# Kernel optimization log

Measured on AMD Instinct MI355X. Metric: run time of the kernel, lower is better.

## Reference

```python
import jax, jax.numpy as jnp
import numpy as np

NEG_SLOPE = 0.01  # torch nn.LeakyReLU default
K_NN = 3          # PyG knn_interpolate default


def lrelu(v):
    return jax.nn.leaky_relu(v, NEG_SLOPE)


def mpl(x, ei, We, be, Wn, bn_):
    # MeshGraphNets-style message passing: edge MLP on [x_src||x_dst],
    # sum-aggregate at dst, node MLP on [x||agg].
    src, dst = ei[0], ei[1]
    m = lrelu(jnp.concatenate([x[src], x[dst]], axis=-1) @ We + be)   # [E, Co]
    agg = jax.ops.segment_sum(m, dst, num_segments=x.shape[0])        # [N, Co]
    return lrelu(jnp.concatenate([x, agg], axis=-1) @ Wn + bn_)


def knn_interpolate(x_c, pos_c, pos_f):
    # PyG knn_interpolate: inverse-squared-distance weighted k-NN average.
    d2 = jnp.sum((pos_f[:, None, :] - pos_c[None, :, :]) ** 2, axis=-1)  # [Nf, Nc]
    neg_d2, idx = jax.lax.top_k(-d2, K_NN)                               # [Nf, k]
    w = 1.0 / (-neg_d2 + 1e-16)
    xg = x_c[idx]                                                        # [Nf, k, C]
    return jnp.sum(w[..., None] * xg, axis=1) / jnp.sum(w, axis=1, keepdims=True)


def batch_norm(x, gamma, beta, eps=1e-5):
    # training-mode BatchNorm over the flattened node dim (PyG BatchNorm)
    mu = x.mean(axis=0)
    var = x.var(axis=0)
    return (x - mu) * jax.lax.rsqrt(var + eps) * gamma + beta


def setup_inputs() -> dict:
    key = jax.random.key(0)
    ks = jax.random.split(key, 20)
    B, Nc, Nf, D = 4, 2048, 8192, 3
    Cin, Cout = 128, 128
    Ch = Cout // 2
    Ec, Ef = 16384, 65536

    def w(k, shape):
        return jax.random.normal(k, shape, jnp.float32) / np.float32(np.sqrt(shape[0]))

    inp = {
        "x": jax.random.normal(ks[0], (B, Nc, Cin), jnp.float32),
        "weights": jax.random.uniform(ks[1], (B, Nc, 1), dtype=jnp.float32),
        "pos": jax.random.uniform(ks[2], (B, Nf, D), dtype=jnp.float32),
        # mpl1: Cin -> Cout//2 (coarse graph)
        "W1e": w(ks[3], (2 * Cin, Ch)), "b1e": jnp.zeros((Ch,), jnp.float32),
        "W1n": w(ks[4], (Cin + Ch, Ch)), "b1n": jnp.zeros((Ch,), jnp.float32),
        # mpl2: Cout//2 -> Cout (fine graph)
        "W2e": w(ks[5], (2 * Ch, Cout)), "b2e": jnp.zeros((Cout,), jnp.float32),
        "W2n": w(ks[6], (Ch + Cout, Cout)), "b2n": jnp.zeros((Cout,), jnp.float32),
        # mpl_skip: Cin -> Cout (fine graph)
        "Wse": w(ks[7], (2 * Cin, Cout)), "bse": jnp.zeros((Cout,), jnp.float32),
        "Wsn": w(ks[8], (Cin + Cout, Cout)), "bsn": jnp.zeros((Cout,), jnp.float32),
        "gamma": jnp.ones((Cout,), jnp.float32),
        "beta": jnp.zeros((Cout,), jnp.float32),
        # mask: indices of coarse nodes inside the fine node set (disjoint per graph)
        "mask": jnp.arange(B * Nc, dtype=jnp.int32).reshape(B, Nc),
        "e_coarse": jax.random.randint(ks[9], (B, 2, Ec), 0, Nc, jnp.int32),
        "e_fine": jax.random.randint(ks[10], (B, 2, Ef), 0, Nf, jnp.int32),
    }
    return inp


def reference(x, weights, pos, W1e, b1e, W1n, b1n, W2e, b2e, W2n, b2n,
              Wse, bse, Wsn, bsn, gamma, beta, mask, e_coarse, e_fine):
    B, Nf, _ = pos.shape

    def per_graph(xg, wg, posg, mg, ec, ef):
        pos_c = posg[mg]                                   # coarse positions
        # skip branch: up-pool then message passing on fine graph
        x_up = knn_interpolate(xg, pos_c, posg)            # [Nf, Cin]
        x_skip = mpl(x_up, ef, Wse, bse, Wsn, bsn)         # [Nf, Cout]
        # main branch: mpl on coarse graph, up-pool, mpl on fine graph
        x1 = mpl(xg, ec, W1e, b1e, W1n, b1n)               # [Nc, Cout//2]
        x1_up = knn_interpolate(x1, pos_c, posg)           # [Nf, Cout//2]
        x2 = mpl(x1_up, ef, W2e, b2e, W2n, b2n)            # [Nf, Cout]
        # Unpool node weights (scatter into zeros at mask rows)
        w_fine = jnp.zeros((Nf, wg.shape[-1]), wg.dtype).at[mg].set(wg)
        return x2 + x_skip, w_fine

    xs, w_fine = jax.vmap(per_graph)(x, weights, pos, mask, e_coarse, e_fine)
    C = xs.shape[-1]
    y = lrelu(batch_norm(xs.reshape(-1, C), gamma, beta)).reshape(xs.shape)
    return y, w_fine
```

## Files before the change

### kernel.cpp

```cpp
#include <hip/hip_runtime.h>
#include <hip/hip_bf16.h>
#include <cfloat>

#define B 4
#define NC 2048
#define NF 8192
#define CIN 128
#define CH 64
#define COUT 128
#define EC 16384
#define EF 65536
#define ZB 256

typedef __attribute__((ext_vector_type(8))) short short8v;
typedef __attribute__((ext_vector_type(4))) float f32x4;

__device__ __forceinline__ ushort f2b(float v) {
    __hip_bfloat16 h = __float2bfloat16(v);
    return *reinterpret_cast<ushort*>(&h);
}
__device__ __forceinline__ float b2f(ushort u) {
    __hip_bfloat16 h = *reinterpret_cast<__hip_bfloat16*>(&u);
    return __bfloat162float(h);
}

__global__ void count_all(const int* __restrict__ ec, const int* __restrict__ ef,
                          const int* __restrict__ mask, const float* __restrict__ pos,
                          int* __restrict__ cntC, int* __restrict__ cntF, int* __restrict__ cntZ) {
    const int b = blockIdx.y, z = blockIdx.z;
    const int i = blockIdx.x * 256 + threadIdx.x;
    if (z == 0) {
        if (i < EC) atomicAdd(&cntC[b * NC + ec[(size_t)b * 2 * EC + EC + i]], 1);
    } else if (z == 1) {
        if (i < EF) atomicAdd(&cntF[b * NF + ef[(size_t)b * 2 * EF + EF + i]], 1);
    } else {
        if (i < NC) {
            int m = mask[b * NC + i];
            float pz = pos[((size_t)b * NF + m) * 3 + 2];
            int zb = min(max((int)(pz * (float)ZB), 0), ZB - 1);
            atomicAdd(&cntZ[b * ZB + zb], 1);
        }
    }
}

template<int N, int OSTR, bool EXTRA>
__device__ __forceinline__ void scan_body(const int* __restrict__ cnt, int* __restrict__ offs,
                                          int* __restrict__ cur, int b, int* part) {
    const int tid = threadIdx.x;
    constexpr int PER = (N + 1023) / 1024;
    int local[PER];
    int s = 0;
    #pragma unroll
    for (int i = 0; i < PER; ++i) {
        int id = tid * PER + i;
        local[i] = s;
        if (id < N) s += cnt[b * N + id];
    }
    part[tid] = s;
    __syncthreads();
    for (int off = 1; off < 1024; off <<= 1) {
        int v = (tid >= off) ? part[tid - off] : 0;
        __syncthreads();
        part[tid] += v;
        __syncthreads();
    }
    int pre = tid ? part[tid - 1] : 0;
    #pragma unroll
    for (int i = 0; i < PER; ++i) {
        int id = tid * PER + i;
        if (id < N) {
            int o = pre + local[i];
            offs[b * OSTR + id] = o;
            cur[b * OSTR + id] = o;
        }
    }
    if (EXTRA && tid == 1023) offs[b * OSTR + N] = part[1023];
}

__global__ __launch_bounds__(1024) void scan_all(
    const int* __restrict__ cntC, int* __restrict__ offC, int* __restrict__ curC,
    const int* __restrict__ cntF, int* __restrict__ offF, int* __restrict__ curF,
    const int* __restrict__ cntZ, int* __restrict__ offZ, int* __restrict__ curZ) {
    __shared__ int part[1024];
    const int cfg = blockIdx.x >> 2;
    const int b = blockIdx.x & 3;
    if (cfg == 0)      scan_body<NC, NC, false>(cntC, offC, curC, b, part);
    else if (cfg == 1) scan_body<NF, NF, false>(cntF, offF, curF, b, part);
    else               scan_body<ZB, ZB + 1, true>(cntZ, offZ, curZ, b, part);
}

__global__ void fill_all(const int* __restrict__ ec, const int* __restrict__ ef,
                         const int* __restrict__ mask, const float* __restrict__ pos,
                         int* __restrict__ curC, int* __restrict__ curF, int* __restrict__ curZ,
                         int* __restrict__ csrC, int* __restrict__ csrF,
                         float4* __restrict__ sposg) {
    const int b = blockIdx.y, z = blockIdx.z;
    const int i = blockIdx.x * 256 + threadIdx.x;
    if (z == 0) {
        if (i < EC) {
            const int* eb = ec + (size_t)b * 2 * EC;
            int src = eb[i], dst = eb[EC + i];
            int p = atomicAdd(&curC[b * NC + dst], 1);
            csrC[(size_t)b * EC + p] = src;
        }
    } else if (z == 1) {
        if (i < EF) {
            const int* eb = ef + (size_t)b * 2 * EF;
            int src = eb[i], dst = eb[EF + i];
            int p = atomicAdd(&curF[b * NF + dst], 1);
            csrF[(size_t)b * EF + p] = src;
        }
    } else {
        if (i < NC) {
            int m = mask[b * NC + i];
            const float* p = pos + ((size_t)b * NF + m) * 3;
            float px = p[0], py = p[1], pz = p[2];
            int zb = min(max((int)(pz * (float)ZB), 0), ZB - 1);
            int slot = atomicAdd(&curZ[b * (ZB + 1) + zb], 1);
            sposg[(size_t)b * NC + slot] = make_float4(px, py, pz, __int_as_float(i));
        }
    }
}

__device__ __forceinline__ void ins3(float d, int c, float& d0, float& d1, float& d2,
                                     int& i0, int& i1, int& i2) {
    bool lt0 = d < d0, lt1 = d < d1, lt2 = d < d2;
    d2 = lt1 ? d1 : (lt2 ? d : d2);  i2 = lt1 ? i1 : (lt2 ? c : i2);
    d1 = lt0 ? d0 : (lt1 ? d : d1);  i1 = lt0 ? i0 : (lt1 ? c : i1);
    d0 = lt0 ? d  : d0;              i0 = lt0 ? c  : i0;
}
__device__ __forceinline__ void merge32(float& d0, float& d1, float& d2,
                                        int& i0, int& i1, int& i2) {
    #pragma unroll
    for (int off = 1; off <= 16; off <<= 1) {
        float od[3]; int oi[3];
        od[0] = __shfl_xor(d0, off); oi[0] = __shfl_xor(i0, off);
        od[1] = __shfl_xor(d1, off); oi[1] = __shfl_xor(i1, off);
        od[2] = __shfl_xor(d2, off); oi[2] = __shfl_xor(i2, off);
        #pragma unroll
        for (int j = 0; j < 3; ++j) ins3(od[j], oi[j], d0, d1, d2, i0, i1, i2);
    }
}

__global__ __launch_bounds__(256) void knn_interp(const float* __restrict__ pos,
                                                  const float4* __restrict__ sposg,
                                                  const int* __restrict__ offZ,
                                                  const float* __restrict__ xc,
                                                  int* __restrict__ idx,
                                                  float* __restrict__ wn,
                                                  ushort* __restrict__ xup) {
    const int b = blockIdx.y;
    const int tid = threadIdx.x;
    const int node = blockIdx.x * 8 + (tid >> 5);
    const int lane = tid & 31;
    const float* pf = pos + ((size_t)b * NF + node) * 3;
    const float px = pf[0], py = pf[1], pz = pf[2];
    const float4* sp = sposg + (size_t)b * NC;
    const int zb = min(max((int)(pz * (float)ZB), 0), ZB - 1);
    const int zlo = max(zb - 32, 0), zhi = min(zb + 32, ZB - 1);
    const int j0 = offZ[b * (ZB + 1) + zlo];
    const int j1 = offZ[b * (ZB + 1) + zhi + 1];
    float d0 = FLT_MAX, d1 = FLT_MAX, d2 = FLT_MAX;
    int i0 = 0, i1 = 0, i2 = 0;
    for (int j = j0 + lane; j < j1; j += 32) {
        float4 s = sp[j];
        float ddx = __fsub_rn(px, s.x);
        float ddy = __fsub_rn(py, s.y);
        float ddz = __fsub_rn(pz, s.z);
        float d = __fadd_rn(__fadd_rn(__fmul_rn(ddx, ddx), __fmul_rn(ddy, ddy)),
                            __fmul_rn(ddz, ddz));
        ins3(d, __float_as_int(s.w), d0, d1, d2, i0, i1, i2);
    }
    merge32(d0, d1, d2, i0, i1, i2);
    float bd = 1e30f;
    if (zlo > 0)      bd = fminf(bd, pz - (float)zlo * (1.0f / ZB));
    if (zhi < ZB - 1) bd = fminf(bd, (float)(zhi + 1) * (1.0f / ZB) - pz);
    bd *= 0.9999f;
    if (__any(d2 > bd * bd)) {
        d0 = d1 = d2 = FLT_MAX; i0 = i1 = i2 = 0;
        for (int j = lane; j < NC; j += 32) {
            float4 s = sp[j];
            float ddx = __fsub_rn(px, s.x);
            float ddy = __fsub_rn(py, s.y);
            float ddz = __fsub_rn(pz, s.z);
            float d = __fadd_rn(__fadd_rn(__fmul_rn(ddx, ddx), __fmul_rn(ddy, ddy)),
                                __fmul_rn(ddz, ddz));
            ins3(d, __float_as_int(s.w), d0, d1, d2, i0, i1, i2);
        }
        merge32(d0, d1, d2, i0, i1, i2);
    }
    float w0 = 1.0f / (d0 + 1e-16f);
    float w1 = 1.0f / (d1 + 1e-16f);
    float w2 = 1.0f / (d2 + 1e-16f);
    float inv = 1.0f / (w0 + w1 + w2);
    w0 *= inv; w1 *= inv; w2 *= inv;
    if (lane == 0) {
        size_t o = ((size_t)b * NF + node) * 3;
        idx[o] = i0; idx[o + 1] = i1; idx[o + 2] = i2;
        wn[o] = w0; wn[o + 1] = w1; wn[o + 2] = w2;
    }
    const float* xb = xc + (size_t)b * NC * CIN;
    float4 a = *(const float4*)&xb[(size_t)i0 * CIN + lane * 4];
    float4 bb = *(const float4*)&xb[(size_t)i1 * CIN + lane * 4];
    float4 cc = *(const float4*)&xb[(size_t)i2 * CIN + lane * 4];
    ushort4 u;
    u.x = f2b(w0 * a.x + w1 * bb.x + w2 * cc.x);
    u.y = f2b(w0 * a.y + w1 * bb.y + w2 * cc.y);
    u.z = f2b(w0 * a.z + w1 * bb.z + w2 * cc.z);
    u.w = f2b(w0 * a.w + w1 * bb.w + w2 * cc.w);
    *(ushort4*)&xup[((size_t)b * NF + node) * CIN + lane * 4] = u;
}

template<int S>
__global__ __launch_bounds__(256) void interp_b16(const float* __restrict__ xc,
                                                  const int* __restrict__ idx,
                                                  const float* __restrict__ wn,
                                                  ushort* __restrict__ out) {
    constexpr int C = 4 << S;
    const int b = blockIdx.y;
    const int node = blockIdx.x * (256 >> S) + (threadIdx.x >> S);
    const int lane = threadIdx.x & ((1 << S) - 1);
    size_t o = ((size_t)b * NF + node) * 3;
    int i0 = idx[o], i1 = idx[o + 1], i2 = idx[o + 2];
    float w0 = wn[o], w1 = wn[o + 1], w2 = wn[o + 2];
    const float* xb = xc + (size_t)b * NC * C;
    float4 a = *(const float4*)&xb[(size_t)i0 * C + lane * 4];
    float4 bb = *(const float4*)&xb[(size_t)i1 * C + lane * 4];
    float4 cc = *(const float4*)&xb[(size_t)i2 * C + lane * 4];
    ushort4 u;
    u.x = f2b(w0 * a.x + w1 * bb.x + w2 * cc.x);
    u.y = f2b(w0 * a.y + w1 * bb.y + w2 * cc.y);
    u.z = f2b(w0 * a.z + w1 * bb.z + w2 * cc.z);
    u.w = f2b(w0 * a.w + w1 * bb.w + w2 * cc.w);
    *(ushort4*)&out[((size_t)b * NF + node) * C + lane * 4] = u;
}

__global__ __launch_bounds__(256) void gemm_kernel(
    const float* __restrict__ A1, int K1, const float* __restrict__ A2, int K2,
    const float* __restrict__ W, const float* __restrict__ bias,
    float* __restrict__ Cmat, int M, int N, int flags,
    long sA1, long sA2, long sC) {
    __shared__ float As[16][64];
    __shared__ float Wsh[16][64];
    const int b = blockIdx.z;
    const int m0 = blockIdx.y * 64, n0 = blockIdx.x * 64;
    const int t = threadIdx.x;
    const int tx = t & 15, ty = t >> 4;
    float acc[4][4] = {};
    int kOff = 0;
    for (int s = 0; s < 2; ++s) {
        const float* A = (s == 0) ? A1 : A2;
        const int K = (s == 0) ? K1 : K2;
        const long sA = (s == 0) ? sA1 : sA2;
        if (A == nullptr || K == 0) continue;
        const float* Ab = A + (size_t)b * sA;
        const int lm = t >> 2;
        const int lk = (t & 3) << 2;
        const int wk = t >> 4;
        const int wng = (t & 15) << 2;
        for (int k0 = 0; k0 < K; k0 += 16) {
            float4 av = *(const float4*)&Ab[(size_t)(m0 + lm) * K + k0 + lk];
            As[lk + 0][lm] = av.x; As[lk + 1][lm] = av.y;
            As[lk + 2][lm] = av.z; As[lk + 3][lm] = av.w;
            float4 wv = *(const float4*)&W[(size_t)(kOff + k0 + wk) * N + n0 + wng];
            *(float4*)&Wsh[wk][wng] = wv;
            __syncthreads();
            #pragma unroll
            for (int k = 0; k < 16; ++k) {
                float4 a4 = *(const float4*)&As[k][ty << 2];
                float4 w4 = *(const float4*)&Wsh[k][tx << 2];
                float aa[4] = {a4.x, a4.y, a4.z, a4.w};
                float ww[4] = {w4.x, w4.y, w4.z, w4.w};
                #pragma unroll
                for (int i = 0; i < 4; ++i)
                    #pragma unroll
                    for (int j = 0; j < 4; ++j)
                        acc[i][j] = fmaf(aa[i], ww[j], acc[i][j]);
            }
            __syncthreads();
        }
        kOff += K;
    }
    float* Cb = Cmat + (size_t)b * sC;
    #pragma unroll
    for (int i = 0; i < 4; ++i) {
        int m = m0 + (ty << 2) + i;
        #pragma unroll
        for (int j = 0; j < 4; ++j) {
            int n = n0 + (tx << 2) + j;
            float v = acc[i][j];
            if (bias) v += bias[n];
            if (flags & 1) v = v > 0.0f ? v : 0.01f * v;
            float* cp = &Cb[(size_t)m * N + n];
            if (flags & 2) v += *cp;
            *cp = v;
        }
    }
}

__global__ __launch_bounds__(256) void gemm_pq64(const float* __restrict__ x,
                                                 const float* __restrict__ W1e,
                                                 float* __restrict__ Pb,
                                                 float* __restrict__ Qb) {
    __shared__ float As[16][64];
    __shared__ float Wsh[16][64];
    const int z = blockIdx.z;
    const int b = z >> 1, pq = z & 1;
    const int m0 = blockIdx.x * 64;
    const float* Ab = x + (size_t)b * NC * CIN;
    const float* W = W1e + pq * CIN * CH;
    float* Cb = (pq ? Qb : Pb) + (size_t)b * NC * CH;
    const int t = threadIdx.x;
    const int tx = t & 15, ty = t >> 4;
    const int lm = t >> 2, lk = (t & 3) << 2;
    const int wk = t >> 4, wng = (t & 15) << 2;
    float acc[4][4] = {};
    for (int k0 = 0; k0 < CIN; k0 += 16) {
        float4 av = *(const float4*)&Ab[(size_t)(m0 + lm) * CIN + k0 + lk];
        As[lk + 0][lm] = av.x; As[lk + 1][lm] = av.y;
        As[lk + 2][lm] = av.z; As[lk + 3][lm] = av.w;
        float4 wv = *(const float4*)&W[(size_t)(k0 + wk) * CH + wng];
        *(float4*)&Wsh[wk][wng] = wv;
        __syncthreads();
        #pragma unroll
        for (int k = 0; k < 16; ++k) {
            float4 a4 = *(const float4*)&As[k][ty << 2];
            float4 w4 = *(const float4*)&Wsh[k][tx << 2];
            float aa[4] = {a4.x, a4.y, a4.z, a4.w};
            float ww[4] = {w4.x, w4.y, w4.z, w4.w};
            #pragma unroll
            for (int i = 0; i < 4; ++i)
                #pragma unroll
                for (int j = 0; j < 4; ++j)
                    acc[i][j] = fmaf(aa[i], ww[j], acc[i][j]);
        }
        __syncthreads();
    }
    #pragma unroll
    for (int i = 0; i < 4; ++i) {
        int m = m0 + (ty << 2) + i;
        #pragma unroll
        for (int j = 0; j < 4; ++j)
            Cb[(size_t)m * CH + (tx << 2) + j] = acc[i][j];
    }
}

#define LDK 40
__device__ __forceinline__ void mfma_seg(const ushort* __restrict__ Ab, int K, int m0,
                                         const ushort* __restrict__ Wt, int ldW, int wcol0,
                                         ushort* As, ushort* Wsm,
                                         int t, int wr, int wc, int fr, int fq,
                                         f32x4 (&acc)[4][4]) {
    const int sr = t >> 2, sk = (t & 3) * 8;
    for (int k0 = 0; k0 < K; k0 += 32) {
        #pragma unroll
        for (int p = 0; p < 2; ++p) {
            int r = sr + p * 64;
            *reinterpret_cast<int4*>(&As[r * LDK + sk]) =
                *reinterpret_cast<const int4*>(&Ab[(size_t)(m0 + r) * K + k0 + sk]);
            *reinterpret_cast<int4*>(&Wsm[r * LDK + sk]) =
                *reinterpret_cast<const int4*>(&Wt[(size_t)r * ldW + wcol0 + k0 + sk]);
        }
        __syncthreads();
        short8v af[4], wf[4];
        #pragma unroll
        for (int m = 0; m < 4; ++m)
            af[m] = *reinterpret_cast<const short8v*>(&As[(wr * 64 + m * 16 + fr) * LDK + fq * 8]);
        #pragma unroll
        for (int n = 0; n < 4; ++n)
            wf[n] = *reinterpret_cast<const short8v*>(&Wsm[(wc * 64 + n * 16 + fr) * LDK + fq * 8]);
        #pragma unroll
        for (int m = 0; m < 4; ++m)
            #pragma unroll
            for (int n = 0; n < 4; ++n)
                acc[m][n] = __builtin_amdgcn_mfma_f32_16x16x32_bf16(af[m], wf[n], acc[m][n], 0, 0, 0);
        __syncthreads();
    }
}

__global__ __launch_bounds__(256) void mfma_pq_both(
    const ushort* __restrict__ x1upb, const ushort* __restrict__ xupb,
    const ushort* __restrict__ W2eT, const ushort* __restrict__ WseT,
    ushort* __restrict__ P2, ushort* __restrict__ Q2,
    ushort* __restrict__ PS, ushort* __restrict__ QS) {
    __shared__ ushort As[128 * LDK];
    __shared__ ushort Wsm[128 * LDK];
    const int t = threadIdx.x;
    const int lane = t & 63, wid = t >> 6;
    const int wr = wid >> 1, wc = wid & 1;
    const int fr = lane & 15, fq = lane >> 4;
    const int z = blockIdx.z;
    const int b = z >> 2, sel = z & 3;
    const int br = sel >> 1, pq = sel & 1;
    const int m0 = blockIdx.x * 128;
    f32x4 acc[4][4];
    #pragma unroll
    for (int m = 0; m < 4; ++m)
        #pragma unroll
        for (int n = 0; n < 4; ++n) acc[m][n] = (f32x4){0.f, 0.f, 0.f, 0.f};
    ushort* outp;
    if (br == 0) {
        mfma_seg(x1upb + (size_t)b * NF * 64, 64, m0, W2eT, 128, pq * 64,
                 As, Wsm, t, wr, wc, fr, fq, acc);
        outp = pq ? Q2 : P2;
    } else {
        mfma_seg(xupb + (size_t)b * NF * 128, 128, m0, WseT, 256, pq * 128,
                 As, Wsm, t, wr, wc, fr, fq, acc);
        outp = pq ? QS : PS;
    }
    ushort* Cb = outp + (size_t)b * NF * 128;
    #pragma unroll
    for (int m = 0; m < 4; ++m)
        #pragma unroll
        for (int n = 0; n < 4; ++n) {
            int col = wc * 64 + n * 16 + fr;
            #pragma unroll
            for (int r = 0; r < 4; ++r) {
                int row = m0 + wr * 64 + m * 16 + fq * 4 + r;
                Cb[(size_t)row * 128 + col] = f2b(acc[m][n][r]);
            }
        }
}

__global__ __launch_bounds__(256) void mfma_node2(
    const ushort* __restrict__ A1, const ushort* __restrict__ A2,
    const ushort* __restrict__ Wt1, const float* __restrict__ bias1,
    const ushort* __restrict__ A3, const ushort* __restrict__ A4,
    const ushort* __restrict__ Wt2, const float* __restrict__ bias2,
    float* __restrict__ y, float* __restrict__ stats) {
    __shared__ ushort As[128 * LDK];
    __shared__ ushort Wsm[128 * LDK];
    const int t = threadIdx.x;
    const int lane = t & 63, wid = t >> 6;
    const int wr = wid >> 1, wc = wid & 1;
    const int fr = lane & 15, fq = lane >> 4;
    const int b = blockIdx.z;
    const int m0 = blockIdx.x * 128;
    f32x4 acc1[4][4], acc2[4][4];
    #pragma unroll
    for (int m = 0; m < 4; ++m)
        #pragma unroll
        for (int n = 0; n < 4; ++n) {
            acc1[m][n] = (f32x4){0.f, 0.f, 0.f, 0.f};
            acc2[m][n] = (f32x4){0.f, 0.f, 0.f, 0.f};
        }
    mfma_seg(A1 + (size_t)b * NF * 64,  64,  m0, Wt1, 192, 0,   As, Wsm, t, wr, wc, fr, fq, acc1);
    mfma_seg(A2 + (size_t)b * NF * 128, 128, m0, Wt1, 192, 64,  As, Wsm, t, wr, wc, fr, fq, acc1);
    mfma_seg(A3 + (size_t)b * NF * 128, 128, m0, Wt2, 256, 0,   As, Wsm, t, wr, wc, fr, fq, acc2);
    mfma_seg(A4 + (size_t)b * NF * 128, 128, m0, Wt2, 256, 128, As, Wsm, t, wr, wc, fr, fq, acc2);
    float* Yb = y + (size_t)b * NF * 128;
    float lsum[4] = {0.f, 0.f, 0.f, 0.f}, lsq[4] = {0.f, 0.f, 0.f, 0.f};
    #pragma unroll
    for (int m = 0; m < 4; ++m)
        #pragma unroll
        for (int n = 0; n < 4; ++n) {
            int col = wc * 64 + n * 16 + fr;
            float bv1 = bias1[col], bv2 = bias2[col];
            #pragma unroll
            for (int r = 0; r < 4; ++r) {
                int row = m0 + wr * 64 + m * 16 + fq * 4 + r;
                float v1 = acc1[m][n][r] + bv1; v1 = v1 > 0.0f ? v1 : 0.01f * v1;
                float v2 = acc2[m][n][r] + bv2; v2 = v2 > 0.0f ? v2 : 0.01f * v2;
                float v = v1 + v2;
                Yb[(size_t)row * 128 + col] = v;
                lsum[n] += v;
                lsq[n] = fmaf(v, v, lsq[n]);
            }
        }
    __syncthreads();
    float* ssum = reinterpret_cast<float*>(As);
    float* ssq  = ssum + 128;
    if (t < 128) { ssum[t] = 0.0f; ssq[t] = 0.0f; }
    __syncthreads();
    #pragma unroll
    for (int n = 0; n < 4; ++n) {
        int col = wc * 64 + n * 16 + fr;
        atomicAdd(&ssum[col], lsum[n]);
        atomicAdd(&ssq[col], lsq[n]);
    }
    __syncthreads();
    if (t < 128) {
        atomicAdd(&stats[t], ssum[t]);
        atomicAdd(&stats[128 + t], ssq[t]);
    }
}

__global__ void conv_wt(const float* __restrict__ W2e, const float* __restrict__ W2n,
                        const float* __restrict__ Wse, const float* __restrict__ Wsn,
                        ushort* __restrict__ W2eT, ushort* __restrict__ W2nT,
                        ushort* __restrict__ WseT, ushort* __restrict__ WsnT) {
    const float* src; ushort* dst; int K2;
    switch (blockIdx.y) {
        case 0: src = W2e; dst = W2eT; K2 = 128; break;
        case 1: src = W2n; dst = W2nT; K2 = 192; break;
        case 2: src = Wse; dst = WseT; K2 = 256; break;
        default: src = Wsn; dst = WsnT; K2 = 256; break;
    }
    int id = blockIdx.x * 256 + threadIdx.x;
    if (id >= K2 * 128) return;
    int n = id & 127, k = id >> 7;
    dst[(size_t)n * K2 + k] = f2b(src[id]);
}

__global__ __launch_bounds__(256) void agg_csr_f32(const float* __restrict__ P,
                                                   const float* __restrict__ Q,
                                                   const float* __restrict__ bias,
                                                   const int* __restrict__ offs,
                                                   const int* __restrict__ counts,
                                                   const int* __restrict__ csr_src,
                                                   float* __restrict__ agg,
                                                   int N, int E) {
    const int b = blockIdx.y;
    const int dst = blockIdx.x * 4 + (threadIdx.x >> 6);
    const int lane = threadIdx.x & 63;
    const float* Pb = P + (size_t)b * N * 64;
    const float* Qb = Q + (size_t)b * N * 64;
    const int start = offs[b * N + dst];
    const int cnt = counts[b * N + dst];
    const int* sl = csr_src + (size_t)b * E + start;
    const float q = Qb[(size_t)dst * 64 + lane] + bias[lane];
    float a = 0.0f;
    for (int i = 0; i < cnt; ++i) {
        int src = sl[i];
        float m = Pb[(size_t)src * 64 + lane] + q; m = m > 0.0f ? m : 0.01f * m;
        a += m;
    }
    agg[(size_t)b * N * 64 + (size_t)dst * 64 + lane] = a;
}

__global__ __launch_bounds__(256) void agg_csr_b16(const ushort* __restrict__ P2,
                                                   const ushort* __restrict__ Q2,
                                                   const float* __restrict__ b2,
                                                   const ushort* __restrict__ PS,
                                                   const ushort* __restrict__ QS,
                                                   const float* __restrict__ bS,
                                                   const int* __restrict__ offs,
                                                   const int* __restrict__ counts,
                                                   const int* __restrict__ csr_src,
                                                   ushort* __restrict__ agg2,
                                                   ushort* __restrict__ aggS) {
    const int lin = blockIdx.x;
    const int pair = lin & 7;
    const int b = pair >> 1, br = pair & 1;
    const int chunk = lin >> 3;
    const ushort* P = br ? PS : P2;
    const ushort* Q = br ? QS : Q2;
    const float* bias = br ? bS : b2;
    ushort* agg = br ? aggS : agg2;
    const int dst = chunk * 4 + (threadIdx.x >> 6);
    const int lane = threadIdx.x & 63;
    const ushort* Pb = P + (size_t)b * NF * 128;
    const ushort* Qb = Q + (size_t)b * NF * 128;
    const int start = offs[b * NF + dst];
    const int cnt = counts[b * NF + dst];
    const int* sl = csr_src + (size_t)b * EF + start;
    const int c0 = lane, c1 = lane + 64;
    const float q0 = b2f(Qb[(size_t)dst * 128 + c0]) + bias[c0];
    const float q1 = b2f(Qb[(size_t)dst * 128 + c1]) + bias[c1];
    float a0 = 0.0f, a1 = 0.0f;
    int i = 0;
    for (; i + 4 <= cnt; i += 4) {
        int s0 = sl[i], s1 = sl[i + 1], s2 = sl[i + 2], s3 = sl[i + 3];
        ushort p00 = Pb[(size_t)s0 * 128 + c0], p01 = Pb[(size_t)s0 * 128 + c1];
        ushort p10 = Pb[(size_t)s1 * 128 + c0], p11 = Pb[(size_t)s1 * 128 + c1];
        ushort p20 = Pb[(size_t)s2 * 128 + c0], p21 = Pb[(size_t)s2 * 128 + c1];
        ushort p30 = Pb[(size_t)s3 * 128 + c0], p31 = Pb[(size_t)s3 * 128 + c1];
        float m;
        m = b2f(p00) + q0; m = m > 0.0f ? m : 0.01f * m; a0 += m;
        m = b2f(p01) + q1; m = m > 0.0f ? m : 0.01f * m; a1 += m;
        m = b2f(p10) + q0; m = m > 0.0f ? m : 0.01f * m; a0 += m;
        m = b2f(p11) + q1; m = m > 0.0f ? m : 0.01f * m; a1 += m;
        m = b2f(p20) + q0; m = m > 0.0f ? m : 0.01f * m; a0 += m;
        m = b2f(p21) + q1; m = m > 0.0f ? m : 0.01f * m; a1 += m;
        m = b2f(p30) + q0; m = m > 0.0f ? m : 0.01f * m; a0 += m;
        m = b2f(p31) + q1; m = m > 0.0f ? m : 0.01f * m; a1 += m;
    }
    for (; i < cnt; ++i) {
        int src = sl[i];
        float m0 = b2f(Pb[(size_t)src * 128 + c0]) + q0; m0 = m0 > 0.0f ? m0 : 0.01f * m0;
        float m1 = b2f(Pb[(size_t)src * 128 + c1]) + q1; m1 = m1 > 0.0f ? m1 : 0.01f * m1;
        a0 += m0; a1 += m1;
    }
    __builtin_nontemporal_store(f2b(a0), &agg[(size_t)b * NF * 128 + (size_t)dst * 128 + c0]);
    __builtin_nontemporal_store(f2b(a1), &agg[(size_t)b * NF * 128 + (size_t)dst * 128 + c1]);
}

__global__ __launch_bounds__(256) void bn_final(float* __restrict__ xs,
                                                const float* __restrict__ stats,
                                                const float* __restrict__ gamma,
                                                const float* __restrict__ beta,
                                                float* __restrict__ wf) {
    const long i = (long)blockIdx.x * 256 + threadIdx.x;
    const long g4 = i * 4;
    const int c = (int)(g4 & (COUT - 1));
    const float invN = 1.0f / (float)(B * NF);
    float4 v = *(float4*)&xs[g4];
    float vv[4] = {v.x, v.y, v.z, v.w};
    #pragma unroll
    for (int k = 0; k < 4; ++k) {
        int ck = c + k;
        float mu = stats[ck] * invN;
        float var = stats[COUT + ck] * invN - mu * mu;
        float t = (vv[k] - mu) * rsqrtf(var + 1e-5f) * gamma[ck] + beta[ck];
        vv[k] = t > 0.0f ? t : 0.01f * t;
    }
    *(float4*)&xs[g4] = make_float4(vv[0], vv[1], vv[2], vv[3]);
    if (i < (long)B * NF / 4)
        *(float4*)&wf[i * 4] = make_float4(0.f, 0.f, 0.f, 0.f);
}

__global__ void wfine_scatter(const float* __restrict__ wts, const int* __restrict__ mask,
                              float* __restrict__ wf) {
    int i = blockIdx.x * 256 + threadIdx.x;
    int b = i / NC;
    wf[(size_t)b * NF + mask[i]] = wts[i];
}

extern "C" void kernel_launch(void* const* d_in, const int* in_sizes, int n_in,
                              void* d_out, int out_size, void* d_ws, size_t ws_size,
                              hipStream_t stream) {
    const float* x    = (const float*)d_in[0];
    const float* wts  = (const float*)d_in[1];
    const float* pos  = (const float*)d_in[2];
    const float* W1e  = (const float*)d_in[3];
    const float* b1e  = (const float*)d_in[4];
    const float* W1n  = (const float*)d_in[5];
    const float* b1n  = (const float*)d_in[6];
    const float* W2e  = (const float*)d_in[7];
    const float* b2e  = (const float*)d_in[8];
    const float* W2n  = (const float*)d_in[9];
    const float* b2n  = (const float*)d_in[10];
    const float* Wse  = (const float*)d_in[11];
    const float* bse  = (const float*)d_in[12];
    const float* Wsn  = (const float*)d_in[13];
    const float* bsn  = (const float*)d_in[14];
    const float* gamma= (const float*)d_in[15];
    const float* beta = (const float*)d_in[16];
    const int*   mask = (const int*)d_in[17];
    const int*   ec   = (const int*)d_in[18];
    const int*   ef   = (const int*)d_in[19];

    float* ws = (float*)d_ws;
    int*    idxb  = (int*)ws;
    float*  wnb   = ws + 98304;
    float4* sposg = (float4*)(ws + 196608);
    float*  x1    = ws + 196608 + 32768;
    float*  PbC   = x1  + (size_t)B * NC * CH;
    float*  QbC   = PbC + (size_t)B * NC * CH;
    float*  aggC  = QbC + (size_t)B * NC * CH;
    float*  stats = aggC+ (size_t)B * NC * CH;
    int* cntC  = (int*)(stats + 256);
    int* cntF  = cntC + B * NC;
    int* cntZ  = cntF + B * NF;
    int* offC  = cntZ + B * ZB;
    int* curC  = offC + B * NC;
    int* offF  = curC + B * NC;
    int* curF  = offF + B * NF;
    int* offZ  = curF + B * NF;
    int* curZ  = offZ + B * (ZB + 1);
    int* csrC  = curZ + B * (ZB + 1);
    int* csrF  = csrC + B * EC;
    size_t foff = (size_t)(csrF + (size_t)B * EF - (int*)ws);
    foff = (foff + 7) & ~(size_t)7;
    ushort* xupb  = (ushort*)(ws + foff);
    ushort* x1upb = xupb  + (size_t)B * NF * 128;
    ushort* P2b   = x1upb + (size_t)B * NF * 64;
    ushort* Q2b   = P2b   + (size_t)B * NF * 128;
    ushort* PSb   = Q2b   + (size_t)B * NF * 128;
    ushort* QSb   = PSb   + (size_t)B * NF * 128;
    ushort* agg2b = QSb   + (size_t)B * NF * 128;
    ushort* aggSb = agg2b + (size_t)B * NF * 128;
    ushort* W2eT  = aggSb + (size_t)B * NF * 128;
    ushort* W2nT  = W2eT  + 128 * 128;
    ushort* WseT  = W2nT  + 128 * 192;
    ushort* WsnT  = WseT  + 128 * 256;

    float* y  = (float*)d_out;
    float* wf = y + (size_t)B * NF * COUT;

    conv_wt<<<dim3(128, 4), 256, 0, stream>>>(W2e, W2n, Wse, Wsn, W2eT, W2nT, WseT, WsnT);
    hipMemsetAsync(stats, 0, 256 * 4 + (size_t)B * (NC + NF + ZB) * 4, stream);
    count_all<<<dim3(EF / 256, B, 3), 256, 0, stream>>>(ec, ef, mask, pos, cntC, cntF, cntZ);
    scan_all<<<dim3(3 * B), 1024, 0, stream>>>(cntC, offC, curC, cntF, offF, curF, cntZ, offZ, curZ);
    fill_all<<<dim3(EF / 256, B, 3), 256, 0, stream>>>(ec, ef, mask, pos, curC, curF, curZ,
                                                       csrC, csrF, sposg);

    knn_interp<<<dim3(NF / 8, B), 256, 0, stream>>>(pos, sposg, offZ, x, idxb, wnb, xupb);

    gemm_pq64<<<dim3(NC / 64, 1, B * 2), 256, 0, stream>>>(x, W1e, PbC, QbC);
    agg_csr_f32<<<dim3(NC / 4, B), 256, 0, stream>>>(
        PbC, QbC, b1e, offC, cntC, csrC, aggC, NC, EC);
    gemm_kernel<<<dim3(1, NC / 64, B), 256, 0, stream>>>(
        x, CIN, aggC, CH, W1n, b1n, x1, NC, CH, 1, (long)NC * CIN, (long)NC * CH, (long)NC * CH);

    interp_b16<4><<<dim3(NF / 16, B), 256, 0, stream>>>(x1, idxb, wnb, x1upb);

    mfma_pq_both<<<dim3(NF / 128, 1, B * 4), 256, 0, stream>>>(
        x1upb, xupb, W2eT, WseT, P2b, Q2b, PSb, QSb);
    agg_csr_b16<<<dim3((NF / 4) * B * 2), 256, 0, stream>>>(
        P2b, Q2b, b2e, PSb, QSb, bse, offF, cntF, csrF, agg2b, aggSb);

    mfma_node2<<<dim3(NF / 128, 1, B), 256, 0, stream>>>(
        x1upb, agg2b, W2nT, b2n, xupb, aggSb, WsnT, bsn, y, stats);

    bn_final<<<dim3((long)B * NF * COUT / 1024), 256, 0, stream>>>(y, stats, gamma, beta, wf);
    wfine_scatter<<<dim3(B * NC / 256), 256, 0, stream>>>(wts, mask, wf);
}
```

Before: 197.2 us.

## Fold weight conversion and w_fine scatter into existing kernels; fuse P/Q GEMMs

Moves the weight transpose/bf16 conversion into an extra z-slice of count_all, and replaces the separate wfine_scatter kernel with an inverse mask map built in fill_all and consumed by bn_final. This removes two kernel launches. The edge-GEMM kernel now computes both the P and Q halves in one block, so each A tile is loaded once instead of twice. The cost is twice the accumulator registers and an extra shared-memory weight buffer, which may lower occupancy. The inverse map assumes mask entries are unique within a graph.

```diff
diff --git a/kernel.cpp b/kernel.cpp
--- a/kernel.cpp
+++ b/kernel.cpp
@@ -26,19 +26,37 @@
 
 __global__ void count_all(const int* __restrict__ ec, const int* __restrict__ ef,
                           const int* __restrict__ mask, const float* __restrict__ pos,
-                          int* __restrict__ cntC, int* __restrict__ cntF, int* __restrict__ cntZ) {
+                          int* __restrict__ cntC, int* __restrict__ cntF, int* __restrict__ cntZ,
+                          int* __restrict__ inv,
+                          const float* __restrict__ W2e, const float* __restrict__ W2n,
+                          const float* __restrict__ Wse, const float* __restrict__ Wsn,
+                          ushort* __restrict__ W2eT, ushort* __restrict__ W2nT,
+                          ushort* __restrict__ WseT, ushort* __restrict__ WsnT) {
     const int b = blockIdx.y, z = blockIdx.z;
     const int i = blockIdx.x * 256 + threadIdx.x;
     if (z == 0) {
         if (i < EC) atomicAdd(&cntC[b * NC + ec[(size_t)b * 2 * EC + EC + i]], 1);
     } else if (z == 1) {
         if (i < EF) atomicAdd(&cntF[b * NF + ef[(size_t)b * 2 * EF + EF + i]], 1);
-    } else {
+        if (i < NF) inv[(size_t)b * NF + i] = -1;
+    } else if (z == 2) {
         if (i < NC) {
             int m = mask[b * NC + i];
             float pz = pos[((size_t)b * NF + m) * 3 + 2];
             int zb = min(max((int)(pz * (float)ZB), 0), ZB - 1);
             atomicAdd(&cntZ[b * ZB + zb], 1);
+        }
+    } else {
+        const float* src; ushort* dst; int K2;
+        switch (b) {
+            case 0: src = W2e; dst = W2eT; K2 = 128; break;
+            case 1: src = W2n; dst = W2nT; K2 = 192; break;
+            case 2: src = Wse; dst = WseT; K2 = 256; break;
+            default: src = Wsn; dst = WsnT; K2 = 256; break;
+        }
+        if (i < K2 * 128) {
+            int n = i & 127, k = i >> 7;
+            dst[(size_t)n * K2 + k] = f2b(src[i]);
         }
     }
 }
@@ -93,7 +111,7 @@
                          const int* __restrict__ mask, const float* __restrict__ pos,
                          int* __restrict__ curC, int* __restrict__ curF, int* __restrict__ curZ,
                          int* __restrict__ csrC, int* __restrict__ csrF,
-                         float4* __restrict__ sposg) {
+                         float4* __restrict__ sposg, int* __restrict__ inv) {
     const int b = blockIdx.y, z = blockIdx.z;
     const int i = blockIdx.x * 256 + threadIdx.x;
     if (z == 0) {
@@ -118,6 +136,7 @@
             int zb = min(max((int)(pz * (float)ZB), 0), ZB - 1);
             int slot = atomicAdd(&curZ[b * (ZB + 1) + zb], 1);
             sposg[(size_t)b * NC + slot] = make_float4(px, py, pz, __int_as_float(i));
+            inv[(size_t)b * NF + m] = b * NC + i;
         }
     }
 }
@@ -378,37 +397,66 @@
     }
 }
 
-__global__ __launch_bounds__(256) void mfma_pq_both(
+__global__ __launch_bounds__(256) void mfma_pq_fused(
     const ushort* __restrict__ x1upb, const ushort* __restrict__ xupb,
     const ushort* __restrict__ W2eT, const ushort* __restrict__ WseT,
     ushort* __restrict__ P2, ushort* __restrict__ Q2,
     ushort* __restrict__ PS, ushort* __restrict__ QS) {
     __shared__ ushort As[128 * LDK];
-    __shared__ ushort Wsm[128 * LDK];
+    __shared__ ushort Ws0[128 * LDK];
+    __shared__ ushort Ws1[128 * LDK];
     const int t = threadIdx.x;
     const int lane = t & 63, wid = t >> 6;
     const int wr = wid >> 1, wc = wid & 1;
     const int fr = lane & 15, fq = lane >> 4;
+    const int sr = t >> 2, sk = (t & 3) * 8;
     const int z = blockIdx.z;
-    const int b = z >> 2, sel = z & 3;
-    const int br = sel >> 1, pq = sel & 1;
+    const int b = z >> 1, br = z & 1;
     const int m0 = blockIdx.x * 128;
-    f32x4 acc[4][4];
+    const ushort* Ab = br ? xupb + (size_t)b * NF * 128 : x1upb + (size_t)b * NF * 64;
+    const int K = br ? 128 : 64;
+    const ushort* Wt = br ? WseT : W2eT;
+    const int ldW = br ? 256 : 128;
+    f32x4 accP[4][4], accQ[4][4];
     #pragma unroll
     for (int m = 0; m < 4; ++m)
         #pragma unroll
-        for (int n = 0; n < 4; ++n) acc[m][n] = (f32x4){0.f, 0.f, 0.f, 0.f};
-    ushort* outp;
-    if (br == 0) {
-        mfma_seg(x1upb + (size_t)b * NF * 64, 64, m0, W2eT, 128, pq * 64,
-                 As, Wsm, t, wr, wc, fr, fq, acc);
-        outp = pq ? Q2 : P2;
-    } else {
-        mfma_seg(xupb + (size_t)b * NF * 128, 128, m0, WseT, 256, pq * 128,
-                 As, Wsm, t, wr, wc, fr, fq, acc);
-        outp = pq ? QS : PS;
-    }
-    ushort* Cb = outp + (size_t)b * NF * 128;
+        for (int n = 0; n < 4; ++n) {
+            accP[m][n] = (f32x4){0.f, 0.f, 0.f, 0.f};
+            accQ[m][n] = (f32x4){0.f, 0.f, 0.f, 0.f};
+        }
+    for (int k0 = 0; k0 < K; k0 += 32) {
+        #pragma unroll
+        for (int p = 0; p < 2; ++p) {
+            int r = sr + p * 64;
+            *reinterpret_cast<int4*>(&As[r * LDK + sk]) =
+                *reinterpret_cast<const int4*>(&Ab[(size_t)(m0 + r) * K + k0 + sk]);
+            *reinterpret_cast<int4*>(&Ws0[r * LDK + sk]) =
+                *reinterpret_cast<const int4*>(&Wt[(size_t)r * ldW + k0 + sk]);
+            *reinterpret_cast<int4*>(&Ws1[r * LDK + sk]) =
+                *reinterpret_cast<const int4*>(&Wt[(size_t)r * ldW + K + k0 + sk]);
+        }
+        __syncthreads();
+        short8v af[4], w0[4], w1[4];
+        #pragma unroll
+        for (int m = 0; m < 4; ++m)
+            af[m] = *reinterpret_cast<const short8v*>(&As[(wr * 64 + m * 16 + fr) * LDK + fq * 8]);
+        #pragma unroll
+        for (int n = 0; n < 4; ++n) {
+            w0[n] = *reinterpret_cast<const short8v*>(&Ws0[(wc * 64 + n * 16 + fr) * LDK + fq * 8]);
+            w1[n] = *reinterpret_cast<const short8v*>(&Ws1[(wc * 64 + n * 16 + fr) * LDK + fq * 8]);
+        }
+        #pragma unroll
+        for (int m = 0; m < 4; ++m)
+            #pragma unroll
+            for (int n = 0; n < 4; ++n) {
+                accP[m][n] = __builtin_amdgcn_mfma_f32_16x16x32_bf16(af[m], w0[n], accP[m][n], 0, 0, 0);
+                accQ[m][n] = __builtin_amdgcn_mfma_f32_16x16x32_bf16(af[m], w1[n], accQ[m][n], 0, 0, 0);
+            }
+        __syncthreads();
+    }
+    ushort* Pb = (br ? PS : P2) + (size_t)b * NF * 128;
+    ushort* Qb = (br ? QS : Q2) + (size_t)b * NF * 128;
     #pragma unroll
     for (int m = 0; m < 4; ++m)
         #pragma unroll
@@ -417,7 +465,8 @@
             #pragma unroll
             for (int r = 0; r < 4; ++r) {
                 int row = m0 + wr * 64 + m * 16 + fq * 4 + r;
-                Cb[(size_t)row * 128 + col] = f2b(acc[m][n][r]);
+                Pb[(size_t)row * 128 + col] = f2b(accP[m][n][r]);
+                Qb[(size_t)row * 128 + col] = f2b(accQ[m][n][r]);
             }
         }
 }
@@ -483,23 +532,6 @@
         atomicAdd(&stats[t], ssum[t]);
         atomicAdd(&stats[128 + t], ssq[t]);
     }
-}
-
-__global__ void conv_wt(const float* __restrict__ W2e, const float* __restrict__ W2n,
-                        const float* __restrict__ Wse, const float* __restrict__ Wsn,
-                        ushort* __restrict__ W2eT, ushort* __restrict__ W2nT,
-                        ushort* __restrict__ WseT, ushort* __restrict__ WsnT) {
-    const float* src; ushort* dst; int K2;
-    switch (blockIdx.y) {
-        case 0: src = W2e; dst = W2eT; K2 = 128; break;
-        case 1: src = W2n; dst = W2nT; K2 = 192; break;
-        case 2: src = Wse; dst = WseT; K2 = 256; break;
-        default: src = Wsn; dst = WsnT; K2 = 256; break;
-    }
-    int id = blockIdx.x * 256 + threadIdx.x;
-    if (id >= K2 * 128) return;
-    int n = id & 127, k = id >> 7;
-    dst[(size_t)n * K2 + k] = f2b(src[id]);
 }
 
 __global__ __launch_bounds__(256) void agg_csr_f32(const float* __restrict__ P,
@@ -589,7 +621,9 @@
                                                 const float* __restrict__ stats,
                                                 const float* __restrict__ gamma,
                                                 const float* __restrict__ beta,
-                                                float* __restrict__ wf) {
+                                                float* __restrict__ wf,
+                                                const float* __restrict__ wts,
+                                                const int* __restrict__ inv) {
     const long i = (long)blockIdx.x * 256 + threadIdx.x;
     const long g4 = i * 4;
     const int c = (int)(g4 & (COUT - 1));
@@ -605,15 +639,10 @@
         vv[k] = t > 0.0f ? t : 0.01f * t;
     }
     *(float4*)&xs[g4] = make_float4(vv[0], vv[1], vv[2], vv[3]);
-    if (i < (long)B * NF / 4)
-        *(float4*)&wf[i * 4] = make_float4(0.f, 0.f, 0.f, 0.f);
-}
-
-__global__ void wfine_scatter(const float* __restrict__ wts, const int* __restrict__ mask,
-                              float* __restrict__ wf) {
-    int i = blockIdx.x * 256 + threadIdx.x;
-    int b = i / NC;
-    wf[(size_t)b * NF + mask[i]] = wts[i];
+    if (i < (long)B * NF) {
+        int iv = inv[i];
+        wf[i] = (iv >= 0) ? wts[iv] : 0.0f;
+    }
 }
 
 extern "C" void kernel_launch(void* const* d_in, const int* in_sizes, int n_in,
@@ -660,7 +689,8 @@
     int* curZ  = offZ + B * (ZB + 1);
     int* csrC  = curZ + B * (ZB + 1);
     int* csrF  = csrC + B * EC;
-    size_t foff = (size_t)(csrF + (size_t)B * EF - (int*)ws);
+    int* invm  = csrF + B * EF;
+    size_t foff = (size_t)(invm + (size_t)B * NF - (int*)ws);
     foff = (foff + 7) & ~(size_t)7;
     ushort* xupb  = (ushort*)(ws + foff);
     ushort* x1upb = xupb  + (size_t)B * NF * 128;
@@ -678,12 +708,13 @@
     float* y  = (float*)d_out;
     float* wf = y + (size_t)B * NF * COUT;
 
-    conv_wt<<<dim3(128, 4), 256, 0, stream>>>(W2e, W2n, Wse, Wsn, W2eT, W2nT, WseT, WsnT);
     hipMemsetAsync(stats, 0, 256 * 4 + (size_t)B * (NC + NF + ZB) * 4, stream);
-    count_all<<<dim3(EF / 256, B, 3), 256, 0, stream>>>(ec, ef, mask, pos, cntC, cntF, cntZ);
+    count_all<<<dim3(EF / 256, B, 4), 256, 0, stream>>>(
+        ec, ef, mask, pos, cntC, cntF, cntZ, invm,
+        W2e, W2n, Wse, Wsn, W2eT, W2nT, WseT, WsnT);
     scan_all<<<dim3(3 * B), 1024, 0, stream>>>(cntC, offC, curC, cntF, offF, curF, cntZ, offZ, curZ);
     fill_all<<<dim3(EF / 256, B, 3), 256, 0, stream>>>(ec, ef, mask, pos, curC, curF, curZ,
-                                                       csrC, csrF, sposg);
+                                                       csrC, csrF, sposg, invm);
 
     knn_interp<<<dim3(NF / 8, B), 256, 0, stream>>>(pos, sposg, offZ, x, idxb, wnb, xupb);
 
@@ -695,7 +726,7 @@
 
     interp_b16<4><<<dim3(NF / 16, B), 256, 0, stream>>>(x1, idxb, wnb, x1upb);
 
-    mfma_pq_both<<<dim3(NF / 128, 1, B * 4), 256, 0, stream>>>(
+    mfma_pq_fused<<<dim3(NF / 128, 1, B * 2), 256, 0, stream>>>(
         x1upb, xupb, W2eT, WseT, P2b, Q2b, PSb, QSb);
     agg_csr_b16<<<dim3((NF / 4) * B * 2), 256, 0, stream>>>(
         P2b, Q2b, b2e, PSb, QSb, bse, offF, cntF, csrF, agg2b, aggSb);
@@ -703,6 +734,5 @@
     mfma_node2<<<dim3(NF / 128, 1, B), 256, 0, stream>>>(
         x1upb, agg2b, W2nT, b2n, xupb, aggSb, WsnT, bsn, y, stats);
 
-    bn_final<<<dim3((long)B * NF * COUT / 1024), 256, 0, stream>>>(y, stats, gamma, beta, wf);
-    wfine_scatter<<<dim3(B * NC / 256), 256, 0, stream>>>(wts, mask, wf);
-}
+    bn_final<<<dim3((long)B * NF * COUT / 1024), 256, 0, stream>>>(y, stats, gamma, beta, wf, wts, invm);
+}
```

After: 198.3 us. About the same (+0.6%).
